# Kernel optimization log

Measured on AMD Instinct MI355X. Metric: run time of the kernel, lower is better.

## Reference

```python
import jax, jax.numpy as jnp
import numpy as np

LN_EPS = 1e-5


def setup_inputs() -> dict:
    key = jax.random.key(0)
    ks = jax.random.split(key, 8)
    N, c_z, H, C = 256, 128, 4, 32
    s = 0.02  # small init scale for stable softmax
    return {
        "z": jax.random.normal(ks[0], (N, N, c_z), dtype=jnp.float32),
        "ln_g": jnp.ones((c_z,), jnp.float32),
        "ln_b": jnp.zeros((c_z,), jnp.float32),
        "Wb": jax.random.normal(ks[1], (c_z, H), dtype=jnp.float32) * s,
        "Wq": jax.random.normal(ks[2], (c_z, H, C), dtype=jnp.float32) * s,
        "Wk": jax.random.normal(ks[3], (c_z, H, C), dtype=jnp.float32) * s,
        "Wv": jax.random.normal(ks[4], (c_z, H, C), dtype=jnp.float32) * s,
        "Wg": jax.random.normal(ks[5], (c_z, H, C), dtype=jnp.float32) * s,
        "bg": jnp.ones((H, C), jnp.float32),
        "Wo": jax.random.normal(ks[6], (H, C, c_z), dtype=jnp.float32) * s,
        "bo": jnp.zeros((c_z,), jnp.float32),
    }


def reference(z, ln_g, ln_b, Wb, Wq, Wk, Wv, Wg, bg, Wo, bo):
    # TriangleAttention, node_type='starting_node' (Algorithm 13).
    # z: (N, N, c_z)
    C = Wq.shape[-1]
    # LayerNorm over c_z
    mu = jnp.mean(z, axis=-1, keepdims=True)
    var = jnp.var(z, axis=-1, keepdims=True)
    x = (z - mu) * jax.lax.rsqrt(var + LN_EPS) * ln_g + ln_b
    # pairwise additive bias: b[h, j, k] = (x @ Wb)[j, k, h]
    b = jnp.einsum('jkz,zh->hjk', x, Wb)
    # per-head projections; attention over second residue axis (-2),
    # first residue axis i acts as batch
    q = jnp.einsum('ijz,zhc->ijhc', x, Wq)
    k = jnp.einsum('ijz,zhc->ijhc', x, Wk)
    v = jnp.einsum('ijz,zhc->ijhc', x, Wv)
    scores = jnp.einsum('iqhc,ikhc->hiqk', q, k) / jnp.sqrt(jnp.asarray(C, x.dtype))
    scores = scores + b[:, None, :, :]  # broadcast bias over batch axis i
    a = jax.nn.softmax(scores, axis=-1)  # (h, i, q, k)
    o = jnp.einsum('hiqk,ikhc->iqhc', a, v)
    g = jax.nn.sigmoid(jnp.einsum('ijz,zhc->ijhc', x, Wg) + bg)
    o = o * g
    out = jnp.einsum('iqhc,hcz->iqz', o, Wo) + bo
    return out
```

## Files before the change

### kernel.cpp

```cpp
#include <hip/hip_runtime.h>
#include <hip/hip_bf16.h>
#include <math.h>


#define NN 256
#define CZ 128

typedef __attribute__((ext_vector_type(8))) short bf16x8;
typedef __attribute__((ext_vector_type(4))) float f32x4;

__device__ __forceinline__ f32x4 mfma16(bf16x8 a, bf16x8 b, f32x4 c) {
  return __builtin_amdgcn_mfma_f32_16x16x32_bf16(a, b, c, 0, 0, 0);
}
__device__ __forceinline__ unsigned short f2bf(float f) {
  unsigned b = __float_as_uint(f);
  return (unsigned short)((b + 0x7FFFu + ((b >> 16) & 1u)) >> 16);
}
__device__ __forceinline__ float bf2f(unsigned short u) { return __uint_as_float((unsigned)u << 16); }
__device__ __forceinline__ unsigned packbf(float a, float b) {
  return (unsigned)f2bf(a) | ((unsigned)f2bf(b) << 16);
}
__device__ __forceinline__ bf16x8 remap_frag(unsigned pk00, unsigned pk01,
                                             unsigned pk10, unsigned pk11,
                                             int srcA, int srcB, bool hi) {
  unsigned a0 = (unsigned)__shfl((int)pk00, srcA);
  unsigned b0 = (unsigned)__shfl((int)pk10, srcA);
  unsigned a1 = (unsigned)__shfl((int)pk01, srcA);
  unsigned b1 = (unsigned)__shfl((int)pk11, srcA);
  unsigned a2 = (unsigned)__shfl((int)pk00, srcB);
  unsigned b2 = (unsigned)__shfl((int)pk10, srcB);
  unsigned a3 = (unsigned)__shfl((int)pk01, srcB);
  unsigned b3 = (unsigned)__shfl((int)pk11, srcB);
  uint4 u;
  u.x = hi ? b0 : a0;
  u.y = hi ? b1 : a1;
  u.z = hi ? b2 : a2;
  u.w = hi ? b3 : a3;
  return *(bf16x8*)&u;
}

__global__ __launch_bounds__(128) void k_prep(const float* __restrict__ Wq, const float* __restrict__ Wk,
                                              const float* __restrict__ Wv, const float* __restrict__ Wg,
                                              const float* __restrict__ Wo, unsigned short* __restrict__ Wt) {
  int sec = blockIdx.y, n = blockIdx.x, t = threadIdx.x;
  const float* s = sec == 0 ? Wq : sec == 1 ? Wk : sec == 2 ? Wv : sec == 3 ? Wg : Wo;
  Wt[(sec * 128 + n) * 128 + t] = f2bf(s[t * 128 + n]);
}

__global__ __launch_bounds__(256) void k_ln(const float* __restrict__ z,
                                            const float* __restrict__ ln_g,
                                            const float* __restrict__ ln_b,
                                            const float* __restrict__ Wb,
                                            unsigned short* __restrict__ xb,
                                            float* __restrict__ bN) {
  int t = threadIdx.x, wave = t >> 6, lane = t & 63;
  int p = blockIdx.x * 64 + wave * 16 + (lane >> 2);
  int q4 = lane & 3;
  const float* src = z + (size_t)p * CZ + q4 * 32;
  float x[32];
  float s = 0.f, sq = 0.f;
#pragma unroll
  for (int e = 0; e < 8; e++) {
    float4 v = *(const float4*)(src + e * 4);
    x[e * 4 + 0] = v.x; x[e * 4 + 1] = v.y; x[e * 4 + 2] = v.z; x[e * 4 + 3] = v.w;
    s += (v.x + v.y) + (v.z + v.w);
    sq += (v.x * v.x + v.y * v.y) + (v.z * v.z + v.w * v.w);
  }
  s += __shfl_xor(s, 1); sq += __shfl_xor(sq, 1);
  s += __shfl_xor(s, 2); sq += __shfl_xor(sq, 2);
  float mean = s * (1.0f / CZ);
  float var = sq * (1.0f / CZ) - mean * mean;
  float rstd = rsqrtf(var + 1e-5f);
  float b0 = 0.f, b1 = 0.f, b2 = 0.f, b3 = 0.f;
  unsigned pk[16];
#pragma unroll
  for (int e = 0; e < 8; e++) {
    float4 gv = *(const float4*)(ln_g + q4 * 32 + e * 4);
    float4 bv = *(const float4*)(ln_b + q4 * 32 + e * 4);
    float x0 = (x[e * 4 + 0] - mean) * rstd * gv.x + bv.x;
    float x1 = (x[e * 4 + 1] - mean) * rstd * gv.y + bv.y;
    float x2 = (x[e * 4 + 2] - mean) * rstd * gv.z + bv.z;
    float x3 = (x[e * 4 + 3] - mean) * rstd * gv.w + bv.w;
    pk[e * 2 + 0] = packbf(x0, x1);
    pk[e * 2 + 1] = packbf(x2, x3);
    int zr = (q4 * 32 + e * 4) * 4;
    float4 w0 = *(const float4*)(Wb + zr);
    float4 w1 = *(const float4*)(Wb + zr + 4);
    float4 w2 = *(const float4*)(Wb + zr + 8);
    float4 w3 = *(const float4*)(Wb + zr + 12);
    b0 += x0 * w0.x + x1 * w1.x + x2 * w2.x + x3 * w3.x;
    b1 += x0 * w0.y + x1 * w1.y + x2 * w2.y + x3 * w3.y;
    b2 += x0 * w0.z + x1 * w1.z + x2 * w2.z + x3 * w3.z;
    b3 += x0 * w0.w + x1 * w1.w + x2 * w2.w + x3 * w3.w;
  }
  unsigned* dst = (unsigned*)(xb + (size_t)p * CZ + q4 * 32);
#pragma unroll
  for (int u = 0; u < 4; u++) ((uint4*)dst)[u] = ((uint4*)pk)[u];
  b0 += __shfl_xor(b0, 1); b1 += __shfl_xor(b1, 1);
  b2 += __shfl_xor(b2, 1); b3 += __shfl_xor(b3, 1);
  b0 += __shfl_xor(b0, 2); b1 += __shfl_xor(b1, 2);
  b2 += __shfl_xor(b2, 2); b3 += __shfl_xor(b3, 2);
  if (q4 == 0) {
    const float L2E = 1.4426950408889634f;
    int j = p >> 8, kk = p & 255;
    bN[0 * 65536 + j * 256 + kk] = b0 * L2E;
    bN[1 * 65536 + j * 256 + kk] = b1 * L2E;
    bN[2 * 65536 + j * 256 + kk] = b2 * L2E;
    bN[3 * 65536 + j * 256 + kk] = b3 * L2E;
  }
}

__global__ __launch_bounds__(256, 3) void k_head(const unsigned short* __restrict__ xb,
                                                 const unsigned short* __restrict__ Wt,
                                                 const float* __restrict__ bN,
                                                 const float* __restrict__ bg,
                                                 unsigned short* __restrict__ og) {
  __shared__ unsigned short ks[256][40];
  __shared__ unsigned short vt[32][264];
  int i = blockIdx.x, h = blockIdx.y;
  int t = threadIdx.x, w = t >> 6, lane = t & 63, l16 = lane & 15, g = lane >> 4;
  const int srcA = l16 + 32 * (g & 1);
  const int srcB = srcA + 16;
  const bool hi = g >= 2;
  const float sc2 = 0.25503486f;

  bf16x8 qa[4];
  unsigned gtp[4][2][2];

  bf16x8 xa[4][4];
#pragma unroll
  for (int mm = 0; mm < 4; mm++)
#pragma unroll
    for (int kt = 0; kt < 4; kt++)
      xa[mm][kt] = *(const bf16x8*)(xb + (size_t)(i * 256 + w * 64 + mm * 16 + l16) * CZ + kt * 32 + g * 8);

  {
    bf16x8 wf[2][4];
#pragma unroll
    for (int n = 0; n < 2; n++)
#pragma unroll
      for (int kt = 0; kt < 4; kt++)
        wf[n][kt] = *(const bf16x8*)(Wt + (size_t)(128 + h * 32 + n * 16 + l16) * CZ + kt * 32 + g * 8);
#pragma unroll
    for (int rh = 0; rh < 2; rh++) {
      f32x4 d[2][2];
#pragma unroll
      for (int m = 0; m < 2; m++)
#pragma unroll
        for (int n = 0; n < 2; n++) d[m][n] = (f32x4){0.f, 0.f, 0.f, 0.f};
#pragma unroll
      for (int kt = 0; kt < 4; kt++)
#pragma unroll
        for (int m = 0; m < 2; m++)
#pragma unroll
          for (int n = 0; n < 2; n++) d[m][n] = mfma16(wf[n][kt], xa[rh * 2 + m][kt], d[m][n]);
#pragma unroll
      for (int m = 0; m < 2; m++)
#pragma unroll
        for (int n = 0; n < 2; n++) {
          ushort4 pk4;
          pk4.x = f2bf(d[m][n][0]); pk4.y = f2bf(d[m][n][1]);
          pk4.z = f2bf(d[m][n][2]); pk4.w = f2bf(d[m][n][3]);
          *(ushort4*)&ks[w * 64 + rh * 32 + m * 16 + l16][n * 16 + g * 4] = pk4;
        }
    }
  }
  {
    bf16x8 wf[2][4];
#pragma unroll
    for (int n = 0; n < 2; n++)
#pragma unroll
      for (int kt = 0; kt < 4; kt++)
        wf[n][kt] = *(const bf16x8*)(Wt + (size_t)(256 + h * 32 + n * 16 + l16) * CZ + kt * 32 + g * 8);
#pragma unroll
    for (int rh = 0; rh < 2; rh++) {
      f32x4 d[2][2];
#pragma unroll
      for (int m = 0; m < 2; m++)
#pragma unroll
        for (int n = 0; n < 2; n++) d[m][n] = (f32x4){0.f, 0.f, 0.f, 0.f};
#pragma unroll
      for (int kt = 0; kt < 4; kt++)
#pragma unroll
        for (int m = 0; m < 2; m++)
#pragma unroll
          for (int n = 0; n < 2; n++) d[m][n] = mfma16(xa[rh * 2 + m][kt], wf[n][kt], d[m][n]);
#pragma unroll
      for (int m = 0; m < 2; m++)
#pragma unroll
        for (int n = 0; n < 2; n++) {
          ushort4 pk4;
          pk4.x = f2bf(d[m][n][0]); pk4.y = f2bf(d[m][n][1]);
          pk4.z = f2bf(d[m][n][2]); pk4.w = f2bf(d[m][n][3]);
          *(ushort4*)&vt[n * 16 + l16][w * 64 + rh * 32 + m * 16 + g * 4] = pk4;
        }
    }
  }
  {
    bf16x8 wf[2][4];
#pragma unroll
    for (int n = 0; n < 2; n++)
#pragma unroll
      for (int kt = 0; kt < 4; kt++)
        wf[n][kt] = *(const bf16x8*)(Wt + (size_t)(0 + h * 32 + n * 16 + l16) * CZ + kt * 32 + g * 8);
#pragma unroll
    for (int rh = 0; rh < 2; rh++) {
      f32x4 d[2][2];
#pragma unroll
      for (int m = 0; m < 2; m++)
#pragma unroll
        for (int n = 0; n < 2; n++) d[m][n] = (f32x4){0.f, 0.f, 0.f, 0.f};
#pragma unroll
      for (int kt = 0; kt < 4; kt++)
#pragma unroll
        for (int m = 0; m < 2; m++)
#pragma unroll
          for (int n = 0; n < 2; n++) d[m][n] = mfma16(wf[n][kt], xa[rh * 2 + m][kt], d[m][n]);
#pragma unroll
      for (int m = 0; m < 2; m++) {
        unsigned pk00 = packbf(d[m][0][0] * sc2, d[m][0][1] * sc2);
        unsigned pk01 = packbf(d[m][0][2] * sc2, d[m][0][3] * sc2);
        unsigned pk10 = packbf(d[m][1][0] * sc2, d[m][1][1] * sc2);
        unsigned pk11 = packbf(d[m][1][2] * sc2, d[m][1][3] * sc2);
        qa[rh * 2 + m] = remap_frag(pk00, pk01, pk10, pk11, srcA, srcB, hi);
      }
    }
  }
  {
    bf16x8 wf[2][4];
#pragma unroll
    for (int n = 0; n < 2; n++)
#pragma unroll
      for (int kt = 0; kt < 4; kt++)
        wf[n][kt] = *(const bf16x8*)(Wt + (size_t)(384 + h * 32 + n * 16 + l16) * CZ + kt * 32 + g * 8);
#pragma unroll
    for (int rh = 0; rh < 2; rh++) {
      f32x4 d[2][2];
#pragma unroll
      for (int m = 0; m < 2; m++)
#pragma unroll
        for (int n = 0; n < 2; n++) d[m][n] = (f32x4){0.f, 0.f, 0.f, 0.f};
#pragma unroll
      for (int kt = 0; kt < 4; kt++)
#pragma unroll
        for (int m = 0; m < 2; m++)
#pragma unroll
          for (int n = 0; n < 2; n++) d[m][n] = mfma16(wf[n][kt], xa[rh * 2 + m][kt], d[m][n]);
#pragma unroll
      for (int n = 0; n < 2; n++) {
        float4 bgv = *(const float4*)(bg + h * 32 + n * 16 + g * 4);
#pragma unroll
        for (int m = 0; m < 2; m++) {
          float s0 = 1.0f / (1.0f + __expf(-(d[m][n][0] + bgv.x)));
          float s1 = 1.0f / (1.0f + __expf(-(d[m][n][1] + bgv.y)));
          float s2 = 1.0f / (1.0f + __expf(-(d[m][n][2] + bgv.z)));
          float s3 = 1.0f / (1.0f + __expf(-(d[m][n][3] + bgv.w)));
          gtp[rh * 2 + m][n][0] = packbf(s0, s1);
          gtp[rh * 2 + m][n][1] = packbf(s2, s3);
        }
      }
    }
  }
  __syncthreads();

  f32x4 oacc[4][2];
  float lsum[4];
#pragma unroll
  for (int qB = 0; qB < 4; qB++) {
    lsum[qB] = 0.f;
    oacc[qB][0] = (f32x4){0.f, 0.f, 0.f, 0.f};
    oacc[qB][1] = (f32x4){0.f, 0.f, 0.f, 0.f};
  }
  const float* bb = bN + (size_t)h * 65536;
  bf16x8 kb[2], vb[2], kbn[2], vbn[2];
#pragma unroll
  for (int n = 0; n < 2; n++) {
    kb[n] = *(const bf16x8*)&ks[0 * 32 + n * 16 + l16][g * 8];
    vb[n] = *(const bf16x8*)&vt[n * 16 + l16][0 * 32 + g * 8];
  }
#pragma unroll 2
  for (int kc = 0; kc < 8; kc++) {
    if (kc < 7) {
#pragma unroll
      for (int n = 0; n < 2; n++) {
        kbn[n] = *(const bf16x8*)&ks[(kc + 1) * 32 + n * 16 + l16][g * 8];
        vbn[n] = *(const bf16x8*)&vt[n * 16 + l16][(kc + 1) * 32 + g * 8];
      }
    }
#pragma unroll
    for (int qB = 0; qB < 4; qB++) {
      int qrow = w * 64 + qB * 16 + l16;
      float4 c0 = *(const float4*)(bb + (size_t)qrow * 256 + kc * 32 + 0 * 16 + g * 4);
      float4 c1 = *(const float4*)(bb + (size_t)qrow * 256 + kc * 32 + 1 * 16 + g * 4);
      f32x4 s0 = mfma16(kb[0], qa[qB], (f32x4){c0.x, c0.y, c0.z, c0.w});
      f32x4 s1 = mfma16(kb[1], qa[qB], (f32x4){c1.x, c1.y, c1.z, c1.w});
      float p0 = exp2f(s0[0]), p1 = exp2f(s0[1]), p2 = exp2f(s0[2]), p3 = exp2f(s0[3]);
      float p4 = exp2f(s1[0]), p5 = exp2f(s1[1]), p6 = exp2f(s1[2]), p7 = exp2f(s1[3]);
      lsum[qB] += ((p0 + p1) + (p2 + p3)) + ((p4 + p5) + (p6 + p7));
      unsigned pk00 = packbf(p0, p1), pk01 = packbf(p2, p3);
      unsigned pk10 = packbf(p4, p5), pk11 = packbf(p6, p7);
      bf16x8 pf = remap_frag(pk00, pk01, pk10, pk11, srcA, srcB, hi);
      oacc[qB][0] = mfma16(vb[0], pf, oacc[qB][0]);
      oacc[qB][1] = mfma16(vb[1], pf, oacc[qB][1]);
    }
    kb[0] = kbn[0]; kb[1] = kbn[1]; vb[0] = vbn[0]; vb[1] = vbn[1];
  }
  __syncthreads();
  unsigned short* myst = &ks[w * 64][0];
#pragma unroll
  for (int qB = 0; qB < 4; qB++) {
    float l = lsum[qB];
    l += __shfl_xor(l, 16);
    l += __shfl_xor(l, 32);
    float inv = 1.0f / l;
#pragma unroll
    for (int nc = 0; nc < 2; nc++) {
      float g0 = bf2f((unsigned short)(gtp[qB][nc][0] & 0xffffu));
      float g1 = bf2f((unsigned short)(gtp[qB][nc][0] >> 16));
      float g2 = bf2f((unsigned short)(gtp[qB][nc][1] & 0xffffu));
      float g3 = bf2f((unsigned short)(gtp[qB][nc][1] >> 16));
      ushort4 pk4;
      pk4.x = f2bf(oacc[qB][nc][0] * inv * g0);
      pk4.y = f2bf(oacc[qB][nc][1] * inv * g1);
      pk4.z = f2bf(oacc[qB][nc][2] * inv * g2);
      pk4.w = f2bf(oacc[qB][nc][3] * inv * g3);
      *(ushort4*)&myst[(qB * 16 + l16) * 40 + nc * 16 + g * 4] = pk4;
    }
  }
#pragma unroll
  for (int e = 0; e < 8; e++) {
    int row = e * 8 + (lane >> 3), chunk = lane & 7;
    *(ushort4*)(og + (size_t)(i * 256 + w * 64 + row) * 128 + h * 32 + chunk * 4) =
        *(const ushort4*)&myst[row * 40 + chunk * 4];
  }
}

__global__ __launch_bounds__(256, 4) void k_out(const unsigned short* __restrict__ og,
                                                const unsigned short* __restrict__ WoT,
                                                const float* __restrict__ bo,
                                                float* __restrict__ out) {
  __shared__ unsigned short ot[128][136];
  int t = threadIdx.x, w = t >> 6, lane = t & 63, l16 = lane & 15, g = lane >> 4;
  int wr = w >> 1, wc = w & 1;
  int pbase = blockIdx.x * 128;
#pragma unroll
  for (int e = 0; e < 8; e++) {
    int idx = e * 256 + t;
    int row = idx >> 4, chunk = idx & 15;
    uint4 v = *(const uint4*)(og + (size_t)(pbase + row) * 128 + chunk * 8);
    *(uint4*)&ot[row][chunk * 8] = v;
  }
  __syncthreads();
  int prow = wr * 64, cbase = wc * 64;
  f32x4 acc[4][4];
#pragma unroll
  for (int m = 0; m < 4; m++)
#pragma unroll
    for (int n = 0; n < 4; n++) acc[m][n] = (f32x4){0.f, 0.f, 0.f, 0.f};
#pragma unroll
  for (int kt = 0; kt < 4; kt++) {
    bf16x8 a[4], b[4];
#pragma unroll
    for (int m = 0; m < 4; m++)
      a[m] = *(const bf16x8*)&ot[prow + m * 16 + l16][kt * 32 + g * 8];
#pragma unroll
    for (int n = 0; n < 4; n++)
      b[n] = *(const bf16x8*)(WoT + (size_t)(cbase + n * 16 + l16) * 128 + kt * 32 + g * 8);
#pragma unroll
    for (int m = 0; m < 4; m++)
#pragma unroll
      for (int n = 0; n < 4; n++) acc[m][n] = mfma16(a[m], b[n], acc[m][n]);
  }
#pragma unroll
  for (int n = 0; n < 4; n++) {
    int zc = cbase + n * 16 + l16;
    float bv = bo[zc];
#pragma unroll
    for (int m = 0; m < 4; m++) {
#pragma unroll
      for (int r = 0; r < 4; r++)
        out[(size_t)(pbase + prow + m * 16 + g * 4 + r) * 128 + zc] = acc[m][n][r] + bv;
    }
  }
}

extern "C" void kernel_launch(void* const* d_in, const int* in_sizes, int n_in,
                              void* d_out, int out_size, void* d_ws, size_t ws_size,
                              hipStream_t stream) {
  const float* z    = (const float*)d_in[0];
  const float* ln_g = (const float*)d_in[1];
  const float* ln_b = (const float*)d_in[2];
  const float* Wb   = (const float*)d_in[3];
  const float* Wq   = (const float*)d_in[4];
  const float* Wk   = (const float*)d_in[5];
  const float* Wv   = (const float*)d_in[6];
  const float* Wg   = (const float*)d_in[7];
  const float* bg   = (const float*)d_in[8];
  const float* Wo   = (const float*)d_in[9];
  const float* bo   = (const float*)d_in[10];
  float* out = (float*)d_out;

  char* ws = (char*)d_ws;
  unsigned short* xb = (unsigned short*)(ws + 0);
  float*          bN = (float*)(ws + 16777216);
  unsigned short* Wt = (unsigned short*)(ws + 17825792);
  unsigned short* og = (unsigned short*)(ws + 17989632);

  k_prep<<<dim3(128, 5), 128, 0, stream>>>(Wq, Wk, Wv, Wg, Wo, Wt);
  k_ln<<<1024, 256, 0, stream>>>(z, ln_g, ln_b, Wb, xb, bN);
  k_head<<<dim3(256, 4), 256, 0, stream>>>(xb, Wt, bN, bg, og);
  k_out<<<512, 256, 0, stream>>>(og, Wt + 512 * 128, bo, out);
}
```

Before: 206.5 us.

## Cut k_head register pressure and store outputs in fragment-native layout

k_head now loads x fragments per 32-row half instead of holding all 16, and drops the K/V double-buffer prefetch in the attention loop. Both changes lower register use so launch bounds can rise from 3 to 4 blocks per SM. The final LDS transpose and its barrier are removed: each wave writes gated outputs straight to global memory in MFMA fragment order. k_out is reworked to gather that layout and scatter it into its shared tile. The risks are exposed LDS latency in the inner loop, more scattered LDS writes in k_out, and possible register spills under the tighter bound.

```diff
diff --git a/kernel.cpp b/kernel.cpp
--- a/kernel.cpp
+++ b/kernel.cpp
@@ -110,11 +110,11 @@
   }
 }
 
-__global__ __launch_bounds__(256, 3) void k_head(const unsigned short* __restrict__ xb,
+__global__ __launch_bounds__(256, 4) void k_head(const unsigned short* __restrict__ xb,
                                                  const unsigned short* __restrict__ Wt,
                                                  const float* __restrict__ bN,
                                                  const float* __restrict__ bg,
-                                                 unsigned short* __restrict__ og) {
+                                                 unsigned short* __restrict__ og2) {
   __shared__ unsigned short ks[256][40];
   __shared__ unsigned short vt[32][264];
   int i = blockIdx.x, h = blockIdx.y;
@@ -127,22 +127,23 @@
   bf16x8 qa[4];
   unsigned gtp[4][2][2];
 
-  bf16x8 xa[4][4];
-#pragma unroll
-  for (int mm = 0; mm < 4; mm++)
-#pragma unroll
-    for (int kt = 0; kt < 4; kt++)
-      xa[mm][kt] = *(const bf16x8*)(xb + (size_t)(i * 256 + w * 64 + mm * 16 + l16) * CZ + kt * 32 + g * 8);
-
-  {
-    bf16x8 wf[2][4];
-#pragma unroll
-    for (int n = 0; n < 2; n++)
+#pragma unroll
+  for (int rh = 0; rh < 2; rh++) {
+    int r0 = w * 64 + rh * 32;
+    bf16x8 xa[2][4];
+#pragma unroll
+    for (int m = 0; m < 2; m++)
 #pragma unroll
       for (int kt = 0; kt < 4; kt++)
-        wf[n][kt] = *(const bf16x8*)(Wt + (size_t)(128 + h * 32 + n * 16 + l16) * CZ + kt * 32 + g * 8);
-#pragma unroll
-    for (int rh = 0; rh < 2; rh++) {
+        xa[m][kt] = *(const bf16x8*)(xb + (size_t)(i * 256 + r0 + m * 16 + l16) * CZ + kt * 32 + g * 8);
+
+    {
+      bf16x8 wf[2][4];
+#pragma unroll
+      for (int n = 0; n < 2; n++)
+#pragma unroll
+        for (int kt = 0; kt < 4; kt++)
+          wf[n][kt] = *(const bf16x8*)(Wt + (size_t)(128 + h * 32 + n * 16 + l16) * CZ + kt * 32 + g * 8);
       f32x4 d[2][2];
 #pragma unroll
       for (int m = 0; m < 2; m++)
@@ -153,7 +154,7 @@
 #pragma unroll
         for (int m = 0; m < 2; m++)
 #pragma unroll
-          for (int n = 0; n < 2; n++) d[m][n] = mfma16(wf[n][kt], xa[rh * 2 + m][kt], d[m][n]);
+          for (int n = 0; n < 2; n++) d[m][n] = mfma16(wf[n][kt], xa[m][kt], d[m][n]);
 #pragma unroll
       for (int m = 0; m < 2; m++)
 #pragma unroll
@@ -161,30 +162,27 @@
           ushort4 pk4;
           pk4.x = f2bf(d[m][n][0]); pk4.y = f2bf(d[m][n][1]);
           pk4.z = f2bf(d[m][n][2]); pk4.w = f2bf(d[m][n][3]);
-          *(ushort4*)&ks[w * 64 + rh * 32 + m * 16 + l16][n * 16 + g * 4] = pk4;
+          *(ushort4*)&ks[r0 + m * 16 + l16][n * 16 + g * 4] = pk4;
         }
     }
-  }
-  {
-    bf16x8 wf[2][4];
-#pragma unroll
-    for (int n = 0; n < 2; n++)
+    {
+      bf16x8 wf[2][4];
+#pragma unroll
+      for (int n = 0; n < 2; n++)
+#pragma unroll
+        for (int kt = 0; kt < 4; kt++)
+          wf[n][kt] = *(const bf16x8*)(Wt + (size_t)(256 + h * 32 + n * 16 + l16) * CZ + kt * 32 + g * 8);
+      f32x4 d[2][2];
+#pragma unroll
+      for (int m = 0; m < 2; m++)
+#pragma unroll
+        for (int n = 0; n < 2; n++) d[m][n] = (f32x4){0.f, 0.f, 0.f, 0.f};
 #pragma unroll
       for (int kt = 0; kt < 4; kt++)
-        wf[n][kt] = *(const bf16x8*)(Wt + (size_t)(256 + h * 32 + n * 16 + l16) * CZ + kt * 32 + g * 8);
-#pragma unroll
-    for (int rh = 0; rh < 2; rh++) {
-      f32x4 d[2][2];
-#pragma unroll
-      for (int m = 0; m < 2; m++)
-#pragma unroll
-        for (int n = 0; n < 2; n++) d[m][n] = (f32x4){0.f, 0.f, 0.f, 0.f};
-#pragma unroll
-      for (int kt = 0; kt < 4; kt++)
 #pragma unroll
         for (int m = 0; m < 2; m++)
 #pragma unroll
-          for (int n = 0; n < 2; n++) d[m][n] = mfma16(xa[rh * 2 + m][kt], wf[n][kt], d[m][n]);
+          for (int n = 0; n < 2; n++) d[m][n] = mfma16(xa[m][kt], wf[n][kt], d[m][n]);
 #pragma unroll
       for (int m = 0; m < 2; m++)
 #pragma unroll
@@ -192,30 +190,27 @@
           ushort4 pk4;
           pk4.x = f2bf(d[m][n][0]); pk4.y = f2bf(d[m][n][1]);
           pk4.z = f2bf(d[m][n][2]); pk4.w = f2bf(d[m][n][3]);
-          *(ushort4*)&vt[n * 16 + l16][w * 64 + rh * 32 + m * 16 + g * 4] = pk4;
+          *(ushort4*)&vt[n * 16 + l16][r0 + m * 16 + g * 4] = pk4;
         }
     }
-  }
-  {
-    bf16x8 wf[2][4];
-#pragma unroll
-    for (int n = 0; n < 2; n++)
+    {
+      bf16x8 wf[2][4];
+#pragma unroll
+      for (int n = 0; n < 2; n++)
+#pragma unroll
+        for (int kt = 0; kt < 4; kt++)
+          wf[n][kt] = *(const bf16x8*)(Wt + (size_t)(0 + h * 32 + n * 16 + l16) * CZ + kt * 32 + g * 8);
+      f32x4 d[2][2];
+#pragma unroll
+      for (int m = 0; m < 2; m++)
+#pragma unroll
+        for (int n = 0; n < 2; n++) d[m][n] = (f32x4){0.f, 0.f, 0.f, 0.f};
 #pragma unroll
       for (int kt = 0; kt < 4; kt++)
-        wf[n][kt] = *(const bf16x8*)(Wt + (size_t)(0 + h * 32 + n * 16 + l16) * CZ + kt * 32 + g * 8);
-#pragma unroll
-    for (int rh = 0; rh < 2; rh++) {
-      f32x4 d[2][2];
-#pragma unroll
-      for (int m = 0; m < 2; m++)
-#pragma unroll
-        for (int n = 0; n < 2; n++) d[m][n] = (f32x4){0.f, 0.f, 0.f, 0.f};
-#pragma unroll
-      for (int kt = 0; kt < 4; kt++)
 #pragma unroll
         for (int m = 0; m < 2; m++)
 #pragma unroll
-          for (int n = 0; n < 2; n++) d[m][n] = mfma16(wf[n][kt], xa[rh * 2 + m][kt], d[m][n]);
+          for (int n = 0; n < 2; n++) d[m][n] = mfma16(wf[n][kt], xa[m][kt], d[m][n]);
 #pragma unroll
       for (int m = 0; m < 2; m++) {
         unsigned pk00 = packbf(d[m][0][0] * sc2, d[m][0][1] * sc2);
@@ -225,27 +220,24 @@
         qa[rh * 2 + m] = remap_frag(pk00, pk01, pk10, pk11, srcA, srcB, hi);
       }
     }
-  }
-  {
-    bf16x8 wf[2][4];
-#pragma unroll
-    for (int n = 0; n < 2; n++)
+    {
+      bf16x8 wf[2][4];
+#pragma unroll
+      for (int n = 0; n < 2; n++)
+#pragma unroll
+        for (int kt = 0; kt < 4; kt++)
+          wf[n][kt] = *(const bf16x8*)(Wt + (size_t)(384 + h * 32 + n * 16 + l16) * CZ + kt * 32 + g * 8);
+      f32x4 d[2][2];
+#pragma unroll
+      for (int m = 0; m < 2; m++)
+#pragma unroll
+        for (int n = 0; n < 2; n++) d[m][n] = (f32x4){0.f, 0.f, 0.f, 0.f};
 #pragma unroll
       for (int kt = 0; kt < 4; kt++)
-        wf[n][kt] = *(const bf16x8*)(Wt + (size_t)(384 + h * 32 + n * 16 + l16) * CZ + kt * 32 + g * 8);
-#pragma unroll
-    for (int rh = 0; rh < 2; rh++) {
-      f32x4 d[2][2];
-#pragma unroll
-      for (int m = 0; m < 2; m++)
-#pragma unroll
-        for (int n = 0; n < 2; n++) d[m][n] = (f32x4){0.f, 0.f, 0.f, 0.f};
-#pragma unroll
-      for (int kt = 0; kt < 4; kt++)
 #pragma unroll
         for (int m = 0; m < 2; m++)
 #pragma unroll
-          for (int n = 0; n < 2; n++) d[m][n] = mfma16(wf[n][kt], xa[rh * 2 + m][kt], d[m][n]);
+          for (int n = 0; n < 2; n++) d[m][n] = mfma16(wf[n][kt], xa[m][kt], d[m][n]);
 #pragma unroll
       for (int n = 0; n < 2; n++) {
         float4 bgv = *(const float4*)(bg + h * 32 + n * 16 + g * 4);
@@ -272,21 +264,13 @@
     oacc[qB][1] = (f32x4){0.f, 0.f, 0.f, 0.f};
   }
   const float* bb = bN + (size_t)h * 65536;
-  bf16x8 kb[2], vb[2], kbn[2], vbn[2];
-#pragma unroll
-  for (int n = 0; n < 2; n++) {
-    kb[n] = *(const bf16x8*)&ks[0 * 32 + n * 16 + l16][g * 8];
-    vb[n] = *(const bf16x8*)&vt[n * 16 + l16][0 * 32 + g * 8];
-  }
 #pragma unroll 2
   for (int kc = 0; kc < 8; kc++) {
-    if (kc < 7) {
-#pragma unroll
-      for (int n = 0; n < 2; n++) {
-        kbn[n] = *(const bf16x8*)&ks[(kc + 1) * 32 + n * 16 + l16][g * 8];
-        vbn[n] = *(const bf16x8*)&vt[n * 16 + l16][(kc + 1) * 32 + g * 8];
-      }
-    }
+    bf16x8 kb[2], vb[2];
+#pragma unroll
+    for (int n = 0; n < 2; n++) kb[n] = *(const bf16x8*)&ks[kc * 32 + n * 16 + l16][g * 8];
+#pragma unroll
+    for (int n = 0; n < 2; n++) vb[n] = *(const bf16x8*)&vt[n * 16 + l16][kc * 32 + g * 8];
 #pragma unroll
     for (int qB = 0; qB < 4; qB++) {
       int qrow = w * 64 + qB * 16 + l16;
@@ -303,10 +287,8 @@
       oacc[qB][0] = mfma16(vb[0], pf, oacc[qB][0]);
       oacc[qB][1] = mfma16(vb[1], pf, oacc[qB][1]);
     }
-    kb[0] = kbn[0]; kb[1] = kbn[1]; vb[0] = vbn[0]; vb[1] = vbn[1];
-  }
-  __syncthreads();
-  unsigned short* myst = &ks[w * 64][0];
+  }
+  unsigned short* myreg = og2 + (size_t)(((i * 4 + h) * 4 + w) * 2048);
 #pragma unroll
   for (int qB = 0; qB < 4; qB++) {
     float l = lsum[qB];
@@ -324,34 +306,41 @@
       pk4.y = f2bf(oacc[qB][nc][1] * inv * g1);
       pk4.z = f2bf(oacc[qB][nc][2] * inv * g2);
       pk4.w = f2bf(oacc[qB][nc][3] * inv * g3);
-      *(ushort4*)&myst[(qB * 16 + l16) * 40 + nc * 16 + g * 4] = pk4;
-    }
-  }
-#pragma unroll
-  for (int e = 0; e < 8; e++) {
-    int row = e * 8 + (lane >> 3), chunk = lane & 7;
-    *(ushort4*)(og + (size_t)(i * 256 + w * 64 + row) * 128 + h * 32 + chunk * 4) =
-        *(const ushort4*)&myst[row * 40 + chunk * 4];
-  }
-}
-
-__global__ __launch_bounds__(256, 4) void k_out(const unsigned short* __restrict__ og,
+      *(ushort4*)(myreg + (qB * 2 + nc) * 256 + lane * 4) = pk4;
+    }
+  }
+}
+
+__global__ __launch_bounds__(256, 4) void k_out(const unsigned short* __restrict__ og2,
                                                 const unsigned short* __restrict__ WoT,
                                                 const float* __restrict__ bo,
                                                 float* __restrict__ out) {
   __shared__ unsigned short ot[128][136];
   int t = threadIdx.x, w = t >> 6, lane = t & 63, l16 = lane & 15, g = lane >> 4;
-  int wr = w >> 1, wc = w & 1;
-  int pbase = blockIdx.x * 128;
+  int i = blockIdx.x >> 1, half = blockIdx.x & 1;
+  int w0 = half * 2;
 #pragma unroll
   for (int e = 0; e < 8; e++) {
     int idx = e * 256 + t;
-    int row = idx >> 4, chunk = idx & 15;
-    uint4 v = *(const uint4*)(og + (size_t)(pbase + row) * 128 + chunk * 8);
-    *(uint4*)&ot[row][chunk * 8] = v;
+    int region = idx >> 8;
+    int h = region >> 1, wl = region & 1;
+    int within = idx & 255;
+    int qBnc = within >> 5;
+    int lpair = within & 31;
+    int qB = qBnc >> 1, nc = qBnc & 1;
+    uint4 v = *(const uint4*)(og2 + (size_t)(((i * 4 + h) * 4 + (w0 + wl)) * 2048 + qBnc * 256 + lpair * 8));
+    int L0 = lpair * 2, L1 = L0 + 1;
+    int q0 = wl * 64 + qB * 16 + (L0 & 15);
+    int q1 = wl * 64 + qB * 16 + (L1 & 15);
+    int c0 = h * 32 + nc * 16 + (L0 >> 4) * 4;
+    int c1 = h * 32 + nc * 16 + (L1 >> 4) * 4;
+    *(uint2*)&ot[q0][c0] = make_uint2(v.x, v.y);
+    *(uint2*)&ot[q1][c1] = make_uint2(v.z, v.w);
   }
   __syncthreads();
+  int wr = w >> 1, wc = w & 1;
   int prow = wr * 64, cbase = wc * 64;
+  int pbase = blockIdx.x * 128;
   f32x4 acc[4][4];
 #pragma unroll
   for (int m = 0; m < 4; m++)
@@ -401,13 +390,13 @@
   float* out = (float*)d_out;
 
   char* ws = (char*)d_ws;
-  unsigned short* xb = (unsigned short*)(ws + 0);
-  float*          bN = (float*)(ws + 16777216);
-  unsigned short* Wt = (unsigned short*)(ws + 17825792);
-  unsigned short* og = (unsigned short*)(ws + 17989632);
+  unsigned short* xb  = (unsigned short*)(ws + 0);
+  float*          bN  = (float*)(ws + 16777216);
+  unsigned short* Wt  = (unsigned short*)(ws + 17825792);
+  unsigned short* og2 = (unsigned short*)(ws + 17989632);
 
   k_prep<<<dim3(128, 5), 128, 0, stream>>>(Wq, Wk, Wv, Wg, Wo, Wt);
   k_ln<<<1024, 256, 0, stream>>>(z, ln_g, ln_b, Wb, xb, bN);
-  k_head<<<dim3(256, 4), 256, 0, stream>>>(xb, Wt, bN, bg, og);
-  k_out<<<512, 256, 0, stream>>>(og, Wt + 512 * 128, bo, out);
-}
+  k_head<<<dim3(256, 4), 256, 0, stream>>>(xb, Wt, bN, bg, og2);
+  k_out<<<512, 256, 0, stream>>>(og2, Wt + 512 * 128, bo, out);
+}
```

Result: slower. 218.6 us (+5.8%).
